# Optimization experiments

Hardware: AMD Instinct MI355X
Metric: run time of the kernel (lower is better)

Reference implementation:

```python
import jax, jax.numpy as jnp
import numpy as np

N_QUBITS = 6
N_LAYERS = 3
DIM = 2 ** N_QUBITS  # 64

# PauliZ sign table: signs[s, q] = +1 if bit q of basis state s is 0 else -1
# (wire 0 is the most-significant bit, matching pennylane default.qubit)
_IDX = np.arange(DIM)
SIGNS = np.stack([1.0 - 2.0 * ((_IDX >> (N_QUBITS - 1 - q)) & 1) for q in range(N_QUBITS)], axis=1).astype(np.float32)  # (64, 6)


def _rx_mat(theta):  # theta: (B,) -> (B,2,2) complex64
    c = jnp.cos(theta / 2).astype(jnp.complex64)
    s = (-1j * jnp.sin(theta / 2)).astype(jnp.complex64)
    return jnp.stack([jnp.stack([c, s], -1), jnp.stack([s, c], -1)], -2)


def _ry_mat(theta):  # theta: (B,) -> (B,2,2) complex64
    c = jnp.cos(theta / 2).astype(jnp.complex64)
    s = jnp.sin(theta / 2).astype(jnp.complex64)
    return jnp.stack([jnp.stack([c, -s], -1), jnp.stack([s, c], -1)], -2)


def _rz_mat(theta):  # theta: (B,) -> (B,2,2) complex64 (diagonal)
    z = jnp.zeros_like(theta).astype(jnp.complex64)
    e0 = jnp.exp(-1j * theta.astype(jnp.complex64) / 2)
    e1 = jnp.exp(1j * theta.astype(jnp.complex64) / 2)
    return jnp.stack([jnp.stack([e0, z], -1), jnp.stack([z, e1], -1)], -2)


def _apply_1q(state, U, w):
    # state: (B, 64); U: (B,2,2) batched or (2,2) shared; gate on wire w
    B = state.shape[0]
    st = state.reshape(B, 2 ** w, 2, 2 ** (N_QUBITS - 1 - w))
    if U.ndim == 3:
        st = jnp.einsum('bij,bajc->baic', U, st)
    else:
        st = jnp.einsum('ij,bajc->baic', U, st)
    return st.reshape(B, DIM)


def _cnot(state, c, t):
    # CNOT with control wire c, target wire t (fixed structure, batched over B)
    B = state.shape[0]
    s = state.reshape((B,) + (2,) * N_QUBITS)
    ac, at = c + 1, t + 1
    s0 = jnp.take(s, 0, axis=ac)
    s1 = jnp.take(s, 1, axis=ac)
    at2 = at - 1 if at > ac else at  # axis shift after removing control axis
    s1 = jnp.flip(s1, axis=at2)      # X on target when control == 1
    s = jnp.stack([s0, s1], axis=ac)
    return s.reshape(B, DIM)


def simulate(x6, q_weights):
    # x6: (B, 6) angles; q_weights: (3, 6). Returns PauliZ expvals (B, 6).
    B = x6.shape[0]
    state = jnp.zeros((B, DIM), dtype=jnp.complex64).at[:, 0].set(1.0)
    # input encoding: RX, RY, RZ on each wire with rolled input angles
    for i in range(N_QUBITS):
        state = _apply_1q(state, _rx_mat(x6[:, i % N_QUBITS]), i)
        state = _apply_1q(state, _ry_mat(x6[:, (i + 1) % N_QUBITS]), i)
        state = _apply_1q(state, _rz_mat(x6[:, (i + 2) % N_QUBITS]), i)
    # variational layers: RY(weights) then ring of CNOTs
    for l in range(N_LAYERS):
        for q in range(N_QUBITS):
            th = q_weights[l, q]
            c = jnp.cos(th / 2).astype(jnp.complex64)
            s = jnp.sin(th / 2).astype(jnp.complex64)
            U = jnp.stack([jnp.stack([c, -s]), jnp.stack([s, c])])  # (2,2)
            state = _apply_1q(state, U, q)
        for q in range(N_QUBITS):
            state = _cnot(state, q, (q + 1) % N_QUBITS)
    probs = (state.real ** 2 + state.imag ** 2)  # (B, 64) float32
    return probs @ jnp.asarray(SIGNS)            # (B, 6)


def setup_inputs() -> dict:
    key = jax.random.key(0)
    k1, k2, k3, k4 = jax.random.split(key, 4)
    B, H = 32768, 1024
    x = jax.random.normal(k1, (B, N_QUBITS), dtype=jnp.float32)
    hx = jax.random.normal(k2, (B, H), dtype=jnp.float32)
    q_weights = jax.random.uniform(k3, (N_LAYERS, N_QUBITS), dtype=jnp.float32, minval=0.0, maxval=2.0 * np.pi)
    bound = 1.0 / np.sqrt(N_QUBITS)
    fc_w = jax.random.uniform(k4, (H, N_QUBITS), dtype=jnp.float32, minval=-bound, maxval=bound)
    fc_b = jax.random.uniform(jax.random.fold_in(k4, 1), (H,), dtype=jnp.float32, minval=-bound, maxval=bound)
    return {"x": x, "hx": hx, "q_weights": q_weights, "fc_w": fc_w, "fc_b": fc_b}


def reference(x, hx, q_weights, fc_w, fc_b):
    q = simulate(x[:, :N_QUBITS], q_weights)      # (B, 6) PauliZ expvals
    return hx + q @ fc_w.T + fc_b                 # residual + linear
```

## Files before the change

### kernel.cpp

```cpp
#include <hip/hip_runtime.h>


#define NQ 6

__global__ __launch_bounds__(256) void qrnn_kernel(
    const float* __restrict__ x,
    const float* __restrict__ hx,
    const float* __restrict__ qw,
    const float* __restrict__ fc_w,
    const float* __restrict__ fc_b,
    float* __restrict__ out,
    int B, int H)
{
    const int tid  = blockIdx.x * blockDim.x + threadIdx.x;
    const int lane = threadIdx.x & 63;
    const int b    = tid >> 6;
    if (b >= B) return;

    float cx[6], sx[6];
    #pragma unroll
    for (int i = 0; i < 6; ++i) {
        float a = x[(size_t)b * 6 + i] * 0.5f;
        __sincosf(a, &sx[i], &cx[i]);
    }

    float re = (lane == 0) ? 1.0f : 0.0f;
    float im = 0.0f;

    #pragma unroll
    for (int i = 0; i < 6; ++i) {
        const int mask = 1 << (5 - i);
        const bool hi = (lane & mask) != 0;
        {
            float c = cx[i], s = sx[i];
            float pre = __shfl_xor(re, mask);
            float pim = __shfl_xor(im, mask);
            float nre = c * re + s * pim;
            float nim = c * im - s * pre;
            re = nre; im = nim;
        }
        {
            int j = (i + 1) % 6;
            float c = cx[j], s = sx[j];
            float pre = __shfl_xor(re, mask);
            float pim = __shfl_xor(im, mask);
            float ss = hi ? s : -s;
            re = c * re + ss * pre;
            im = c * im + ss * pim;
        }
        {
            int j = (i + 2) % 6;
            float c = cx[j], s = sx[j];
            float ss = hi ? s : -s;
            float nre = c * re - ss * im;
            float nim = c * im + ss * re;
            re = nre; im = nim;
        }
    }

    int src = lane;
    #pragma unroll
    for (int q = 5; q >= 0; --q) {
        int cb = 5 - q;
        int tb = 5 - ((q + 1) % 6);
        src ^= ((src >> cb) & 1) << tb;
    }

    #pragma unroll
    for (int l = 0; l < 3; ++l) {
        #pragma unroll
        for (int q = 0; q < 6; ++q) {
            float th = qw[l * 6 + q] * 0.5f;
            float c, s;
            __sincosf(th, &s, &c);
            const int mask = 1 << (5 - q);
            float pre = __shfl_xor(re, mask);
            float pim = __shfl_xor(im, mask);
            float ss = (lane & mask) ? s : -s;
            re = c * re + ss * pre;
            im = c * im + ss * pim;
        }
        re = __shfl(re, src);
        im = __shfl(im, src);
    }

    const float p = re * re + im * im;
    float q6[6];
    #pragma unroll
    for (int j = 0; j < 6; ++j) {
        float v = (lane & (1 << (5 - j))) ? -p : p;
        #pragma unroll
        for (int m = 1; m < 64; m <<= 1) v += __shfl_xor(v, m);
        q6[j] = v;
    }

    const float4* hx4 = (const float4*)(hx + (size_t)b * H);
    float4*       ot4 = (float4*)(out + (size_t)b * H);
    const float4* w4  = (const float4*)fc_w;
    const float4* bb4 = (const float4*)fc_b;
    const int nChunks = H >> 8;
    for (int k = 0; k < nChunks; ++k) {
        int h4 = k * 64 + lane;
        float4 hv = hx4[h4];
        float4 bv = bb4[h4];
        int wb = h4 * 6;
        float4 a0 = w4[wb + 0], a1 = w4[wb + 1], a2 = w4[wb + 2];
        float4 a3 = w4[wb + 3], a4 = w4[wb + 4], a5 = w4[wb + 5];
        float4 r;
        r.x = hv.x + bv.x + q6[0]*a0.x + q6[1]*a0.y + q6[2]*a0.z + q6[3]*a0.w + q6[4]*a1.x + q6[5]*a1.y;
        r.y = hv.y + bv.y + q6[0]*a1.z + q6[1]*a1.w + q6[2]*a2.x + q6[3]*a2.y + q6[4]*a2.z + q6[5]*a2.w;
        r.z = hv.z + bv.z + q6[0]*a3.x + q6[1]*a3.y + q6[2]*a3.z + q6[3]*a3.w + q6[4]*a4.x + q6[5]*a4.y;
        r.w = hv.w + bv.w + q6[0]*a4.z + q6[1]*a4.w + q6[2]*a5.x + q6[3]*a5.y + q6[4]*a5.z + q6[5]*a5.w;
        ot4[h4] = r;
    }
}

extern "C" void kernel_launch(void* const* d_in, const int* in_sizes, int n_in,
                              void* d_out, int out_size, void* d_ws, size_t ws_size,
                              hipStream_t stream) {
    const float* x    = (const float*)d_in[0];
    const float* hx   = (const float*)d_in[1];
    const float* qw   = (const float*)d_in[2];
    const float* fc_w = (const float*)d_in[3];
    const float* fc_b = (const float*)d_in[4];
    float* out = (float*)d_out;

    const int B = in_sizes[0] / NQ;
    const int H = in_sizes[4];

    const int threads = 256;
    const int blocks  = (B * 64 + threads - 1) / threads;
    qrnn_kernel<<<blocks, threads, 0, stream>>>(x, hx, qw, fc_w, fc_b, out, B, H);
}
```

Baseline: 282.1 us.

## Split into per-thread statevector simulation kernel and row-blocked epilogue kernel

Replaces the one-wavefront-per-sample shuffle-based simulation with one thread per sample that holds the full 64-amplitude statevector in registers, using compile-time gate indexing and a constexpr CNOT-ring permutation. The PauliZ results go to workspace, and a separate epilogue kernel processes 16 rows per block, reusing fc_w and fc_b loads across rows. This removes the cross-lane shuffles and reductions and the redundant per-row weight loads. In exchange it needs very high register use (128+ floats per thread, launch bounds of 64 threads), which may spill, adds a second launch, and leaves only 512 small blocks for the simulation.

```diff
diff --git a/kernel.cpp b/kernel.cpp
--- a/kernel.cpp
+++ b/kernel.cpp
@@ -2,116 +2,154 @@
 
 
 #define NQ 6
+#define DIM 64
 
-__global__ __launch_bounds__(256) void qrnn_kernel(
+struct Perm { int v[DIM]; };
+constexpr Perm make_perm() {
+    Perm p{};
+    for (int s = 0; s < DIM; ++s) {
+        int src = s;
+        for (int q = 5; q >= 0; --q) {
+            int cb = 5 - q;
+            int tb = 5 - ((q + 1) % 6);
+            src ^= ((src >> cb) & 1) << tb;
+        }
+        p.v[s] = src;
+    }
+    return p;
+}
+constexpr Perm PS = make_perm();
+
+template<int BB>
+__device__ __forceinline__ void rx_gate(float* sr, float* si, float c, float sn) {
+    constexpr int m = 1 << BB;
+    #pragma unroll
+    for (int p = 0; p < 32; ++p) {
+        const int s0 = ((p & ~(m - 1)) << 1) | (p & (m - 1));
+        const int s1 = s0 | m;
+        float a0r = sr[s0], a0i = si[s0], a1r = sr[s1], a1i = si[s1];
+        sr[s0] = c * a0r + sn * a1i;
+        si[s0] = c * a0i - sn * a1r;
+        sr[s1] = c * a1r + sn * a0i;
+        si[s1] = c * a1i - sn * a0r;
+    }
+}
+
+template<int BB>
+__device__ __forceinline__ void ry_gate(float* sr, float* si, float c, float sn) {
+    constexpr int m = 1 << BB;
+    #pragma unroll
+    for (int p = 0; p < 32; ++p) {
+        const int s0 = ((p & ~(m - 1)) << 1) | (p & (m - 1));
+        const int s1 = s0 | m;
+        float a0r = sr[s0], a0i = si[s0], a1r = sr[s1], a1i = si[s1];
+        sr[s0] = c * a0r - sn * a1r;
+        si[s0] = c * a0i - sn * a1i;
+        sr[s1] = sn * a0r + c * a1r;
+        si[s1] = sn * a0i + c * a1i;
+    }
+}
+
+template<int BB>
+__device__ __forceinline__ void rz_gate(float* sr, float* si, float c, float sn) {
+    constexpr int m = 1 << BB;
+    #pragma unroll
+    for (int s = 0; s < DIM; ++s) {
+        float r = sr[s], i2 = si[s];
+        if (s & m) { sr[s] = c * r - sn * i2;  si[s] = c * i2 + sn * r; }
+        else       { sr[s] = c * r + sn * i2;  si[s] = c * i2 - sn * r; }
+    }
+}
+
+__device__ __forceinline__ void cnot_ring(float* sr, float* si) {
+    float tr[DIM], ti[DIM];
+    #pragma unroll
+    for (int s = 0; s < DIM; ++s) { tr[s] = sr[PS.v[s]]; ti[s] = si[PS.v[s]]; }
+    #pragma unroll
+    for (int s = 0; s < DIM; ++s) { sr[s] = tr[s]; si[s] = ti[s]; }
+}
+
+__global__ __launch_bounds__(64, 1) void qrnn_sim_kernel(
     const float* __restrict__ x,
+    const float* __restrict__ qw,
+    float* __restrict__ q6,
+    int B)
+{
+    const int b = blockIdx.x * 64 + threadIdx.x;
+    if (b >= B) return;
+
+    float cx[6], sx[6];
+    #pragma unroll
+    for (int i = 0; i < 6; ++i)
+        __sincosf(x[(size_t)b * 6 + i] * 0.5f, &sx[i], &cx[i]);
+
+    float sr[DIM], si[DIM];
+    #pragma unroll
+    for (int s = 0; s < DIM; ++s) { sr[s] = (s == 0) ? 1.0f : 0.0f; si[s] = 0.0f; }
+
+    #define ENC_WIRE(i) \
+        rx_gate<5-(i)>(sr, si, cx[(i)],       sx[(i)]); \
+        ry_gate<5-(i)>(sr, si, cx[((i)+1)%6], sx[((i)+1)%6]); \
+        rz_gate<5-(i)>(sr, si, cx[((i)+2)%6], sx[((i)+2)%6]);
+    ENC_WIRE(0) ENC_WIRE(1) ENC_WIRE(2) ENC_WIRE(3) ENC_WIRE(4) ENC_WIRE(5)
+    #undef ENC_WIRE
+
+    #define VAR_GATE(l, q) { \
+        float c, s2; __sincosf(qw[(l)*6+(q)] * 0.5f, &s2, &c); \
+        ry_gate<5-(q)>(sr, si, c, s2); }
+    #define VAR_LAYER(l) \
+        VAR_GATE(l,0) VAR_GATE(l,1) VAR_GATE(l,2) \
+        VAR_GATE(l,3) VAR_GATE(l,4) VAR_GATE(l,5) \
+        cnot_ring(sr, si);
+    VAR_LAYER(0) VAR_LAYER(1) VAR_LAYER(2)
+    #undef VAR_LAYER
+    #undef VAR_GATE
+
+    float q[6] = {0.f, 0.f, 0.f, 0.f, 0.f, 0.f};
+    #pragma unroll
+    for (int s = 0; s < DIM; ++s) {
+        float p = sr[s] * sr[s] + si[s] * si[s];
+        #pragma unroll
+        for (int j = 0; j < 6; ++j)
+            q[j] += (s & (1 << (5 - j))) ? -p : p;
+    }
+    #pragma unroll
+    for (int j = 0; j < 6; ++j) q6[(size_t)b * 6 + j] = q[j];
+}
+
+#define EPI_ROWS 16
+
+__global__ __launch_bounds__(256) void qrnn_epi_kernel(
     const float* __restrict__ hx,
-    const float* __restrict__ qw,
+    const float* __restrict__ q6,
     const float* __restrict__ fc_w,
     const float* __restrict__ fc_b,
     float* __restrict__ out,
     int B, int H)
 {
-    const int tid  = blockIdx.x * blockDim.x + threadIdx.x;
-    const int lane = threadIdx.x & 63;
-    const int b    = tid >> 6;
-    if (b >= B) return;
-
-    float cx[6], sx[6];
-    #pragma unroll
-    for (int i = 0; i < 6; ++i) {
-        float a = x[(size_t)b * 6 + i] * 0.5f;
-        __sincosf(a, &sx[i], &cx[i]);
-    }
-
-    float re = (lane == 0) ? 1.0f : 0.0f;
-    float im = 0.0f;
-
-    #pragma unroll
-    for (int i = 0; i < 6; ++i) {
-        const int mask = 1 << (5 - i);
-        const bool hi = (lane & mask) != 0;
-        {
-            float c = cx[i], s = sx[i];
-            float pre = __shfl_xor(re, mask);
-            float pim = __shfl_xor(im, mask);
-            float nre = c * re + s * pim;
-            float nim = c * im - s * pre;
-            re = nre; im = nim;
-        }
-        {
-            int j = (i + 1) % 6;
-            float c = cx[j], s = sx[j];
-            float pre = __shfl_xor(re, mask);
-            float pim = __shfl_xor(im, mask);
-            float ss = hi ? s : -s;
-            re = c * re + ss * pre;
-            im = c * im + ss * pim;
-        }
-        {
-            int j = (i + 2) % 6;
-            float c = cx[j], s = sx[j];
-            float ss = hi ? s : -s;
-            float nre = c * re - ss * im;
-            float nim = c * im + ss * re;
-            re = nre; im = nim;
-        }
-    }
-
-    int src = lane;
-    #pragma unroll
-    for (int q = 5; q >= 0; --q) {
-        int cb = 5 - q;
-        int tb = 5 - ((q + 1) % 6);
-        src ^= ((src >> cb) & 1) << tb;
-    }
-
-    #pragma unroll
-    for (int l = 0; l < 3; ++l) {
-        #pragma unroll
-        for (int q = 0; q < 6; ++q) {
-            float th = qw[l * 6 + q] * 0.5f;
-            float c, s;
-            __sincosf(th, &s, &c);
-            const int mask = 1 << (5 - q);
-            float pre = __shfl_xor(re, mask);
-            float pim = __shfl_xor(im, mask);
-            float ss = (lane & mask) ? s : -s;
-            re = c * re + ss * pre;
-            im = c * im + ss * pim;
-        }
-        re = __shfl(re, src);
-        im = __shfl(im, src);
-    }
-
-    const float p = re * re + im * im;
-    float q6[6];
-    #pragma unroll
-    for (int j = 0; j < 6; ++j) {
-        float v = (lane & (1 << (5 - j))) ? -p : p;
-        #pragma unroll
-        for (int m = 1; m < 64; m <<= 1) v += __shfl_xor(v, m);
-        q6[j] = v;
-    }
-
-    const float4* hx4 = (const float4*)(hx + (size_t)b * H);
-    float4*       ot4 = (float4*)(out + (size_t)b * H);
-    const float4* w4  = (const float4*)fc_w;
-    const float4* bb4 = (const float4*)fc_b;
-    const int nChunks = H >> 8;
-    for (int k = 0; k < nChunks; ++k) {
-        int h4 = k * 64 + lane;
-        float4 hv = hx4[h4];
-        float4 bv = bb4[h4];
-        int wb = h4 * 6;
+    const int H4 = H >> 2;
+    const int b0 = blockIdx.x * EPI_ROWS;
+    for (int h4 = threadIdx.x; h4 < H4; h4 += blockDim.x) {
+        const float4* w4 = (const float4*)fc_w;
+        const int wb = h4 * 6;
         float4 a0 = w4[wb + 0], a1 = w4[wb + 1], a2 = w4[wb + 2];
         float4 a3 = w4[wb + 3], a4 = w4[wb + 4], a5 = w4[wb + 5];
-        float4 r;
-        r.x = hv.x + bv.x + q6[0]*a0.x + q6[1]*a0.y + q6[2]*a0.z + q6[3]*a0.w + q6[4]*a1.x + q6[5]*a1.y;
-        r.y = hv.y + bv.y + q6[0]*a1.z + q6[1]*a1.w + q6[2]*a2.x + q6[3]*a2.y + q6[4]*a2.z + q6[5]*a2.w;
-        r.z = hv.z + bv.z + q6[0]*a3.x + q6[1]*a3.y + q6[2]*a3.z + q6[3]*a3.w + q6[4]*a4.x + q6[5]*a4.y;
-        r.w = hv.w + bv.w + q6[0]*a4.z + q6[1]*a4.w + q6[2]*a5.x + q6[3]*a5.y + q6[4]*a5.z + q6[5]*a5.w;
-        ot4[h4] = r;
+        float4 bv = ((const float4*)fc_b)[h4];
+        #pragma unroll
+        for (int r = 0; r < EPI_ROWS; ++r) {
+            const int b = b0 + r;
+            if (b >= B) break;
+            const float* qb = q6 + (size_t)b * 6;
+            float q0 = qb[0], q1 = qb[1], q2 = qb[2];
+            float q3 = qb[3], q4 = qb[4], q5 = qb[5];
+            float4 hv = ((const float4*)(hx + (size_t)b * H))[h4];
+            float4 rres;
+            rres.x = hv.x + bv.x + q0*a0.x + q1*a0.y + q2*a0.z + q3*a0.w + q4*a1.x + q5*a1.y;
+            rres.y = hv.y + bv.y + q0*a1.z + q1*a1.w + q2*a2.x + q3*a2.y + q4*a2.z + q5*a2.w;
+            rres.z = hv.z + bv.z + q0*a3.x + q1*a3.y + q2*a3.z + q3*a3.w + q4*a4.x + q5*a4.y;
+            rres.w = hv.w + bv.w + q0*a4.z + q1*a4.w + q2*a5.x + q3*a5.y + q4*a5.z + q5*a5.w;
+            ((float4*)(out + (size_t)b * H))[h4] = rres;
+        }
     }
 }
 
@@ -128,7 +166,9 @@
     const int B = in_sizes[0] / NQ;
     const int H = in_sizes[4];
 
-    const int threads = 256;
-    const int blocks  = (B * 64 + threads - 1) / threads;
-    qrnn_kernel<<<blocks, threads, 0, stream>>>(x, hx, qw, fc_w, fc_b, out, B, H);
+    float* q6 = (float*)d_ws;
+
+    qrnn_sim_kernel<<<(B + 63) / 64, 64, 0, stream>>>(x, qw, q6, B);
+    qrnn_epi_kernel<<<(B + EPI_ROWS - 1) / EPI_ROWS, 256, 0, stream>>>(
+        hx, q6, fc_w, fc_b, out, B, H);
 }
```

New measurement: 267.9 us. -5.0%, faster.
